# Optimization experiments

Measured on AMD Instinct MI355X. Metric: run time of the kernel, lower is better.

The kernel has to match this reference:

```python
import jax, jax.numpy as jnp
import numpy as np

N = 50000
E = 800000
NEG_SLOPE = 0.2
BN_EPS = 1e-5


def _bn(x, g, b, m, v):
    # BatchNorm1d in eval mode (running stats)
    return (x - m) * (g * jax.lax.rsqrt(v + BN_EPS)) + b


def _gat_conv(x, src, dst, W, a_src, a_dst, bias, heads, hid):
    n = x.shape[0]
    h = (x @ W).reshape(n, heads, hid)                      # [N,H,D]
    s_src = jnp.sum(h * a_src, axis=-1)                     # [N,H]
    s_dst = jnp.sum(h * a_dst, axis=-1)                     # [N,H]
    score = jax.nn.leaky_relu(s_src[src] + s_dst[dst], NEG_SLOPE)  # [E,H]
    # segment softmax over incoming edges of each dst node, per head
    mx = jax.ops.segment_max(score, dst, num_segments=n)
    ex = jnp.exp(score - mx[dst])
    sm = jax.ops.segment_sum(ex, dst, num_segments=n)
    alpha = ex / sm[dst]                                    # [E,H]
    msg = h[src] * alpha[:, :, None]                        # [E,H,D]
    out = jax.ops.segment_sum(msg, dst, num_segments=n)     # [N,H,D]
    return out.reshape(n, heads * hid) + bias


def setup_inputs() -> dict:
    key = jax.random.key(0)
    ks = jax.random.split(key, 16)
    d_in, heads, hid = 64, 8, 32
    wdim = heads * hid  # 256
    inp = {
        "x": jax.random.normal(ks[0], (N, d_in), jnp.float32),
        "edge_index": jax.random.randint(ks[1], (2, E), 0, N, jnp.int32),
        "bn1_g": jnp.ones((d_in,), jnp.float32),
        "bn1_b": jnp.zeros((d_in,), jnp.float32),
        "bn1_m": jnp.zeros((d_in,), jnp.float32),
        "bn1_v": jnp.ones((d_in,), jnp.float32),
        "W1": jax.random.normal(ks[2], (d_in, wdim), jnp.float32) * (1.0 / np.sqrt(d_in)),
        "a1_src": jax.random.normal(ks[3], (heads, hid), jnp.float32) * 0.1,
        "a1_dst": jax.random.normal(ks[4], (heads, hid), jnp.float32) * 0.1,
        "b1": jnp.zeros((wdim,), jnp.float32),
        "bn2_g": jnp.ones((wdim,), jnp.float32),
        "bn2_b": jnp.zeros((wdim,), jnp.float32),
        "bn2_m": jnp.zeros((wdim,), jnp.float32),
        "bn2_v": jnp.ones((wdim,), jnp.float32),
        "W2": jax.random.normal(ks[5], (wdim, wdim), jnp.float32) * (1.0 / np.sqrt(wdim)),
        "a2_src": jax.random.normal(ks[6], (heads, hid), jnp.float32) * 0.1,
        "a2_dst": jax.random.normal(ks[7], (heads, hid), jnp.float32) * 0.1,
        "b2": jnp.zeros((wdim,), jnp.float32),
        "bn3_g": jnp.ones((wdim,), jnp.float32),
        "bn3_b": jnp.zeros((wdim,), jnp.float32),
        "bn3_m": jnp.zeros((wdim,), jnp.float32),
        "bn3_v": jnp.ones((wdim,), jnp.float32),
        "skip_W": jax.random.normal(ks[8], (d_in, wdim), jnp.float32) * (1.0 / np.sqrt(d_in)),
        "skip_b": jnp.zeros((wdim,), jnp.float32),
        "p1_W": jax.random.normal(ks[9], (wdim, hid), jnp.float32) * (1.0 / np.sqrt(wdim)),
        "p1_b": jnp.zeros((hid,), jnp.float32),
        "p2_W": jax.random.normal(ks[10], (hid, 1), jnp.float32) * (1.0 / np.sqrt(hid)),
        "p2_b": jnp.zeros((1,), jnp.float32),
    }
    return inp


def reference(x, edge_index, bn1_g, bn1_b, bn1_m, bn1_v, W1, a1_src, a1_dst, b1,
              bn2_g, bn2_b, bn2_m, bn2_v, W2, a2_src, a2_dst, b2,
              bn3_g, bn3_b, bn3_m, bn3_v, skip_W, skip_b, p1_W, p1_b, p2_W, p2_b):
    heads, hid = 8, 32
    n = x.shape[0]
    # add self loops once (PyG GATConv default add_self_loops=True)
    loops = jnp.arange(n, dtype=edge_index.dtype)
    src = jnp.concatenate([edge_index[0], loops])
    dst = jnp.concatenate([edge_index[1], loops])

    x_in = x
    h = _bn(x, bn1_g, bn1_b, bn1_m, bn1_v)
    h = jax.nn.elu(_gat_conv(h, src, dst, W1, a1_src, a1_dst, b1, heads, hid))
    h = _bn(h, bn2_g, bn2_b, bn2_m, bn2_v)
    h = jax.nn.elu(_gat_conv(h, src, dst, W2, a2_src, a2_dst, b2, heads, hid))
    h = _bn(h, bn3_g, bn3_b, bn3_m, bn3_v)
    h = h + (x_in @ skip_W + skip_b)
    h = jax.nn.relu(h @ p1_W + p1_b)
    return h @ p2_W + p2_b  # [N, 1]
```

## Files before the change

### kernel.cpp

```cpp
#include <hip/hip_runtime.h>
#include <hip/hip_bf16.h>
#include <math.h>
#include <stdint.h>

#define HID 256
#define HEADS 8
#define BN_EPS 1e-5f
#define NEG 0.2f
#define WCAP 96
#define SEPT 8
#define SCHUNK (256 * SEPT)

typedef _Float16 hv8 __attribute__((ext_vector_type(8)));
typedef float f32x4 __attribute__((ext_vector_type(4)));

__device__ __forceinline__ float lrelu(float x) { return x > 0.f ? x : NEG * x; }
__device__ __forceinline__ float eluf(float x)  { return x > 0.f ? x : expm1f(x); }

__device__ __forceinline__ unsigned short f2h(float f) {
    _Float16 h = (_Float16)f;
    union { _Float16 h; unsigned short u; } c; c.h = h;
    return c.u;
}
__device__ __forceinline__ float h2f(unsigned short u) {
    union { unsigned short u; _Float16 h; } c; c.u = u;
    return (float)c.h;
}
__device__ __forceinline__ unsigned int pk2h(float lo, float hi) {
    return (unsigned int)f2h(lo) | ((unsigned int)f2h(hi) << 16);
}

#define FMAMIX_LO(acc, pk, al) \
    asm("v_fma_mix_f32 %0, %1, %2, %0 op_sel:[0,0,0] op_sel_hi:[1,0,0]" \
        : "+v"(acc) : "v"(pk), "v"(al))
#define FMAMIX_HI(acc, pk, al) \
    asm("v_fma_mix_f32 %0, %1, %2, %0 op_sel:[1,0,0] op_sel_hi:[1,0,0]" \
        : "+v"(acc) : "v"(pk), "v"(al))


__global__ __launch_bounds__(256) void degree_kernel(const int* __restrict__ ei,
                                                     int* __restrict__ deg,
                                                     int E, int EE) {
    int e = blockIdx.x * 256 + threadIdx.x;
    if (e >= EE) return;
    int d = (e < E) ? ei[E + e] : (e - E);
    atomicAdd(&deg[d], 1);
}

__global__ __launch_bounds__(256) void scan1_kernel(const int* __restrict__ deg,
                                                    int* __restrict__ bsum, int N) {
    __shared__ int part[256];
    int t = threadIdx.x;
    int base = blockIdx.x * SCHUNK + t * SEPT;
    int s = 0;
    if (base + SEPT <= N) {
        int4 a = *(const int4*)&deg[base];
        int4 c = *(const int4*)&deg[base + 4];
        s = a.x + a.y + a.z + a.w + c.x + c.y + c.z + c.w;
    } else {
#pragma unroll
        for (int i = 0; i < SEPT; ++i) {
            int j = base + i;
            if (j < N) s += deg[j];
        }
    }
    part[t] = s;
    __syncthreads();
    for (int d = 128; d > 0; d >>= 1) {
        if (t < d) part[t] += part[t + d];
        __syncthreads();
    }
    if (t == 0) bsum[blockIdx.x] = part[0];
}

__global__ __launch_bounds__(256) void scan2_kernel(int* __restrict__ bsum,
                                                    int* __restrict__ offs,
                                                    int nb, int N) {
    __shared__ int part[256];
    int t = threadIdx.x;
    int v = (t < nb) ? bsum[t] : 0;
    part[t] = v;
    __syncthreads();
    for (int d = 1; d < 256; d <<= 1) {
        int o = (t >= d) ? part[t - d] : 0;
        __syncthreads();
        part[t] += o;
        __syncthreads();
    }
    if (t < nb) bsum[t] = part[t] - v;
    if (t == 255) offs[N] = part[255];
}

__global__ __launch_bounds__(256) void scan3_kernel(const int* __restrict__ deg,
                                                    const int* __restrict__ bsum,
                                                    int* __restrict__ offs, int N) {
    __shared__ int part[256];
    int t = threadIdx.x;
    int base = blockIdx.x * SCHUNK + t * SEPT;
    int loc[SEPT];
    int s = 0;
#pragma unroll
    for (int i = 0; i < SEPT; ++i) {
        int j = base + i;
        int d = (j < N) ? deg[j] : 0;
        loc[i] = s;
        s += d;
    }
    part[t] = s;
    __syncthreads();
    for (int d = 1; d < 256; d <<= 1) {
        int o = (t >= d) ? part[t - d] : 0;
        __syncthreads();
        part[t] += o;
        __syncthreads();
    }
    int ex = part[t] - s + bsum[blockIdx.x];
#pragma unroll
    for (int i = 0; i < SEPT; ++i) {
        int j = base + i;
        if (j < N) offs[j] = ex + loc[i];
    }
}

__global__ __launch_bounds__(256) void scatter_kernel(const int* __restrict__ ei,
                                                      const int* __restrict__ offs,
                                                      int* __restrict__ cur,
                                                      int* __restrict__ csr_src,
                                                      int E, int EE) {
    int e = blockIdx.x * 256 + threadIdx.x;
    if (e >= EE) return;
    int s = (e < E) ? ei[e] : (e - E);
    int d = (e < E) ? ei[E + e] : (e - E);
    int pos = offs[d] + atomicAdd(&cur[d], 1);
    csr_src[pos] = s;
}

__device__ __forceinline__ void wfrag_body(const float* __restrict__ W,
                                           const float* __restrict__ g,
                                           const float* __restrict__ v,
                                           unsigned short* __restrict__ frag,
                                           int tile, int l) {
    int ct = tile & 15, kt = tile >> 4;
    int c = ct * 16 + (l & 15);
    int k0 = kt * 32 + (l >> 4) * 8;
    float val[8];
#pragma unroll
    for (int j = 0; j < 8; ++j) {
        float s = g[k0 + j] * rsqrtf(v[k0 + j] + BN_EPS);
        val[j] = W[(size_t)(k0 + j) * HID + c] * s;
    }
    uint4 o;
    o.x = pk2h(val[0], val[1]);
    o.y = pk2h(val[2], val[3]);
    o.z = pk2h(val[4], val[5]);
    o.w = pk2h(val[6], val[7]);
    *(uint4*)&frag[((size_t)tile * 64 + l) * 8] = o;
}

__global__ __launch_bounds__(256) void prep_kernel(
    const float* __restrict__ W1, const float* __restrict__ bn1_g,
    const float* __restrict__ bn1_b, const float* __restrict__ bn1_m,
    const float* __restrict__ bn1_v,
    const float* __restrict__ W2, const float* __restrict__ bn2_g,
    const float* __restrict__ bn2_b, const float* __restrict__ bn2_m,
    const float* __restrict__ bn2_v,
    const float* __restrict__ g3, const float* __restrict__ b3,
    const float* __restrict__ m3, const float* __restrict__ v3,
    const float* __restrict__ skip_W, const float* __restrict__ skip_b,
    const float* __restrict__ p1_W, const float* __restrict__ p1_b,
    unsigned short* __restrict__ wf1, unsigned short* __restrict__ wf2,
    unsigned short* __restrict__ hf, float* __restrict__ c1,
    float* __restrict__ c2, float* __restrict__ cp) {
    int b = blockIdx.x;
    int tid = threadIdx.x;
    int sub = tid >> 6, l = tid & 63;

    if (b < 8) {
        wfrag_body(W1, bn1_g, bn1_v, wf1, b * 4 + sub, l);
    } else if (b < 40) {
        wfrag_body(W2, bn2_g, bn2_v, wf2, (b - 8) * 4 + sub, l);
    } else if (b < 45) {
        int tile = (b - 40) * 4 + sub;
        int mt = tile & 1, kt = tile >> 1;
        int j = mt * 16 + (l & 15);
        int k0 = kt * 32 + (l >> 4) * 8;
        float val[8];
#pragma unroll
        for (int jj = 0; jj < 8; ++jj) {
            int c = k0 + jj;
            if (c < HID) {
                float s3 = g3[c] * rsqrtf(v3[c] + BN_EPS);
                val[jj] = s3 * p1_W[c * 32 + j];
            } else {
                float acc = 0.f;
                for (int cc = 0; cc < HID; ++cc)
                    acc = fmaf(skip_W[(size_t)(c - HID) * HID + cc],
                               p1_W[cc * 32 + j], acc);
                val[jj] = acc;
            }
        }
        uint4 o;
        o.x = pk2h(val[0], val[1]);
        o.y = pk2h(val[2], val[3]);
        o.z = pk2h(val[4], val[5]);
        o.w = pk2h(val[6], val[7]);
        *(uint4*)&hf[((size_t)tile * 64 + l) * 8] = o;
    } else if (b == 45) {
        float acc = 0.f;
        for (int k = 0; k < 64; ++k) {
            float s = bn1_g[k] * rsqrtf(bn1_v[k] + BN_EPS);
            acc = fmaf(bn1_b[k] - bn1_m[k] * s, W1[(size_t)k * HID + tid], acc);
        }
        c1[tid] = acc;
    } else if (b == 46) {
        float acc = 0.f;
        for (int k = 0; k < HID; ++k) {
            float s = bn2_g[k] * rsqrtf(bn2_v[k] + BN_EPS);
            acc = fmaf(bn2_b[k] - bn2_m[k] * s, W2[(size_t)k * HID + tid], acc);
        }
        c2[tid] = acc;
    } else {
        if (tid < 32) {
            float acc = p1_b[tid];
            for (int c = 0; c < HID; ++c) {
                float s3 = g3[c] * rsqrtf(v3[c] + BN_EPS);
                acc = fmaf(b3[c] - m3[c] * s3 + skip_b[c], p1_W[c * 32 + tid], acc);
            }
            cp[tid] = acc;
        }
    }
}

template <int K, bool F16IN>
__global__ __launch_bounds__(256) void gemm_mfma(
    const float* __restrict__ inf, const unsigned short* __restrict__ inh,
    const unsigned short* __restrict__ wfrag, const float* __restrict__ cvec,
    const float* __restrict__ a_src, const float* __restrict__ a_dst,
    unsigned short* __restrict__ h, float* __restrict__ s_src,
    float* __restrict__ s_dst, int N) {
    constexpr int KT = K / 32;
    constexpr int OPR = K / 8;
    __shared__ unsigned short xfrag[KT * 4 * 64 * 8];
    int tid = threadIdx.x;
    int w = tid >> 6, l = tid & 63;
    int gg = l >> 4, li = l & 15;
    int base = blockIdx.x * 64;

    for (int id = tid; id < 64 * OPR; id += 256) {
        int r = id / OPR, o = id % OPR;
        int node = min(base + r, N - 1);
        uint4 pkv;
        if constexpr (F16IN) {
            pkv = *(const uint4*)&inh[(size_t)node * K + o * 8];
        } else {
            const float* p = &inf[(size_t)node * K + o * 8];
            float4 f0 = *(const float4*)p;
            float4 f1 = *(const float4*)(p + 4);
            pkv.x = pk2h(f0.x, f0.y);
            pkv.y = pk2h(f0.z, f0.w);
            pkv.z = pk2h(f1.x, f1.y);
            pkv.w = pk2h(f1.z, f1.w);
        }
        int kt = o >> 2, og = o & 3, nt = r >> 4;
        *(uint4*)&xfrag[(((kt * 4 + nt) * 64) + (r & 15) + 16 * og) * 8] = pkv;
    }
    __syncthreads();

    f32x4 acc[4][4];
#pragma unroll
    for (int mm = 0; mm < 4; ++mm) {
        float4 cv = *(const float4*)&cvec[64 * w + 16 * mm + 4 * gg];
#pragma unroll
        for (int nn = 0; nn < 4; ++nn) {
            acc[mm][nn][0] = cv.x; acc[mm][nn][1] = cv.y;
            acc[mm][nn][2] = cv.z; acc[mm][nn][3] = cv.w;
        }
    }

    for (int ks = 0; ks < KT; ++ks) {
        hv8 a[4], b[4];
#pragma unroll
        for (int mm = 0; mm < 4; ++mm)
            a[mm] = *(const hv8*)&wfrag[((size_t)(ks * 16 + w * 4 + mm) * 64 + l) * 8];
#pragma unroll
        for (int nn = 0; nn < 4; ++nn)
            b[nn] = *(const hv8*)&xfrag[((ks * 4 + nn) * 64 + l) * 8];
#pragma unroll
        for (int mm = 0; mm < 4; ++mm)
#pragma unroll
            for (int nn = 0; nn < 4; ++nn)
                acc[mm][nn] = __builtin_amdgcn_mfma_f32_16x16x32_f16(
                    a[mm], b[nn], acc[mm][nn], 0, 0, 0);
    }

    float svp[4][2], sdp[4][2];
#pragma unroll
    for (int nn = 0; nn < 4; ++nn) { svp[nn][0]=0.f; svp[nn][1]=0.f; sdp[nn][0]=0.f; sdp[nn][1]=0.f; }

#pragma unroll
    for (int mm = 0; mm < 4; ++mm) {
        int cb = 64 * w + 16 * mm + 4 * gg;
        float4 as4 = *(const float4*)&a_src[cb];
        float4 ad4 = *(const float4*)&a_dst[cb];
        int hp = mm >> 1;
#pragma unroll
        for (int nn = 0; nn < 4; ++nn) {
            f32x4 A = acc[mm][nn];
            svp[nn][hp] += A[0]*as4.x + A[1]*as4.y + A[2]*as4.z + A[3]*as4.w;
            sdp[nn][hp] += A[0]*ad4.x + A[1]*ad4.y + A[2]*ad4.z + A[3]*ad4.w;
            int node = base + 16 * nn + li;
            if (node < N) {
                ushort4 pkv;
                pkv.x = f2h(A[0]); pkv.y = f2h(A[1]);
                pkv.z = f2h(A[2]); pkv.w = f2h(A[3]);
                *(ushort4*)&h[(size_t)node * HID + cb] = pkv;
            }
        }
    }
#pragma unroll
    for (int nn = 0; nn < 4; ++nn)
#pragma unroll
        for (int hp = 0; hp < 2; ++hp) {
            svp[nn][hp] += __shfl_xor(svp[nn][hp], 16);
            svp[nn][hp] += __shfl_xor(svp[nn][hp], 32);
            sdp[nn][hp] += __shfl_xor(sdp[nn][hp], 16);
            sdp[nn][hp] += __shfl_xor(sdp[nn][hp], 32);
        }
    if (gg == 0) {
#pragma unroll
        for (int nn = 0; nn < 4; ++nn) {
            int node = base + 16 * nn + li;
            if (node < N) {
#pragma unroll
                for (int hp = 0; hp < 2; ++hp) {
                    s_src[node * HEADS + 2 * w + hp] = svp[nn][hp];
                    s_dst[node * HEADS + 2 * w + hp] = sdp[nn][hp];
                }
            }
        }
    }
}

__global__ __launch_bounds__(256) void agg_kernel(
    const unsigned short* __restrict__ h, const float* __restrict__ s_src,
    const float* __restrict__ s_dst, const int* __restrict__ offs,
    const int* __restrict__ csr_src, const float* __restrict__ bias,
    unsigned short* __restrict__ outp, int N) {
    __shared__ float al_lds[4][WCAP][8];
    __shared__ int   u_lds[4][WCAP];
    __shared__ float mi_lds[4][16];
    int tid = threadIdx.x;
    int w = tid >> 6, l = tid & 63;
    int vtx = blockIdx.x * 4 + w;
    if (vtx >= N) return;
    int beg = offs[vtx], end = offs[vtx + 1];
    int deg = end - beg;
    int dc = min(deg, WCAP);

    int headA = l & 7, slot = l >> 3;
    float sdv = s_dst[vtx * HEADS + headA];

    float m = -3.0e38f;
    for (int e = slot; e < deg; e += 8) {
        int u = csr_src[beg + e];
        float sc = lrelu(s_src[u * HEADS + headA] + sdv);
        if (e < WCAP) {
            if (headA == 0) u_lds[w][e] = u;
            al_lds[w][e][headA] = sc;
        }
        m = fmaxf(m, sc);
    }
    m = fmaxf(m, __shfl_xor(m, 8));
    m = fmaxf(m, __shfl_xor(m, 16));
    m = fmaxf(m, __shfl_xor(m, 32));

    float s = 0.f;
    for (int e = slot; e < dc; e += 8) {
        float p = __expf(al_lds[w][e][headA] - m);
        al_lds[w][e][headA] = p;
        s += p;
    }
    for (int e = WCAP + slot; e < deg; e += 8) {
        int u = csr_src[beg + e];
        s += __expf(lrelu(s_src[u * HEADS + headA] + sdv) - m);
    }
    s += __shfl_xor(s, 8);
    s += __shfl_xor(s, 16);
    s += __shfl_xor(s, 32);
    if (slot == 0) {
        mi_lds[w][headA] = m;
        mi_lds[w][8 + headA] = 1.f / s;
    }
    __builtin_amdgcn_wave_barrier();

    int grp = l >> 5, gl = l & 31;
    int hd = gl >> 2;
    float a0 = 0.f, a1 = 0.f, a2 = 0.f, a3 = 0.f;
    float a4 = 0.f, a5 = 0.f, a6 = 0.f, a7 = 0.f;
#pragma unroll 2
    for (int e = grp; e < dc; e += 2) {
        int u = u_lds[w][e];
        float al = al_lds[w][e][hd];
        uint4 hv = *(const uint4*)&h[(size_t)u * HID + 8 * gl];
        FMAMIX_LO(a0, hv.x, al); FMAMIX_HI(a1, hv.x, al);
        FMAMIX_LO(a2, hv.y, al); FMAMIX_HI(a3, hv.y, al);
        FMAMIX_LO(a4, hv.z, al); FMAMIX_HI(a5, hv.z, al);
        FMAMIX_LO(a6, hv.w, al); FMAMIX_HI(a7, hv.w, al);
    }
    if (deg > WCAP) {
        float mh = mi_lds[w][hd];
        float sdh = s_dst[vtx * HEADS + hd];
        for (int e = WCAP + grp; e < deg; e += 2) {
            int u = csr_src[beg + e];
            float al = __expf(lrelu(s_src[u * HEADS + hd] + sdh) - mh);
            uint4 hv = *(const uint4*)&h[(size_t)u * HID + 8 * gl];
            FMAMIX_LO(a0, hv.x, al); FMAMIX_HI(a1, hv.x, al);
            FMAMIX_LO(a2, hv.y, al); FMAMIX_HI(a3, hv.y, al);
            FMAMIX_LO(a4, hv.z, al); FMAMIX_HI(a5, hv.z, al);
            FMAMIX_LO(a6, hv.w, al); FMAMIX_HI(a7, hv.w, al);
        }
    }
    a0 += __shfl_xor(a0, 32); a1 += __shfl_xor(a1, 32);
    a2 += __shfl_xor(a2, 32); a3 += __shfl_xor(a3, 32);
    a4 += __shfl_xor(a4, 32); a5 += __shfl_xor(a5, 32);
    a6 += __shfl_xor(a6, 32); a7 += __shfl_xor(a7, 32);
    if (grp == 0) {
        float inv = mi_lds[w][8 + hd];
        float4 b0 = *(const float4*)&bias[8 * gl];
        float4 b1 = *(const float4*)&bias[8 * gl + 4];
        uint4 ov;
        ov.x = pk2h(eluf(a0 * inv + b0.x), eluf(a1 * inv + b0.y));
        ov.y = pk2h(eluf(a2 * inv + b0.z), eluf(a3 * inv + b0.w));
        ov.z = pk2h(eluf(a4 * inv + b1.x), eluf(a5 * inv + b1.y));
        ov.w = pk2h(eluf(a6 * inv + b1.z), eluf(a7 * inv + b1.w));
        *(uint4*)&outp[(size_t)vtx * HID + 8 * gl] = ov;
    }
}

__global__ __launch_bounds__(256) void final_mfma(
    const unsigned short* __restrict__ t_in, const float* __restrict__ x,
    const unsigned short* __restrict__ hf, const float* __restrict__ cp,
    const float* __restrict__ p2_W, const float* __restrict__ p2_b,
    float* __restrict__ outp, int N) {
    constexpr int KT = 10;
    __shared__ unsigned short xfrag[KT * 4 * 64 * 8];
    int tid = threadIdx.x;
    int w = tid >> 6, l = tid & 63;
    int gg = l >> 4, li = l & 15;
    int base = blockIdx.x * 64;

    for (int id = tid; id < 64 * 40; id += 256) {
        int r = id / 40, o = id % 40;
        int node = min(base + r, N - 1);
        uint4 pkv;
        if (o < 32) {
            pkv = *(const uint4*)&t_in[(size_t)node * HID + o * 8];
        } else {
            const float* p = &x[(size_t)node * 64 + (o - 32) * 8];
            float4 f0 = *(const float4*)p;
            float4 f1 = *(const float4*)(p + 4);
            pkv.x = pk2h(f0.x, f0.y);
            pkv.y = pk2h(f0.z, f0.w);
            pkv.z = pk2h(f1.x, f1.y);
            pkv.w = pk2h(f1.z, f1.w);
        }
        int kt = o >> 2, og = o & 3, nt = r >> 4;
        *(uint4*)&xfrag[(((kt * 4 + nt) * 64) + (r & 15) + 16 * og) * 8] = pkv;
    }
    __syncthreads();

    f32x4 acc[2];
#pragma unroll
    for (int mt = 0; mt < 2; ++mt) {
        float4 cv = *(const float4*)&cp[mt * 16 + 4 * gg];
        acc[mt][0] = cv.x; acc[mt][1] = cv.y; acc[mt][2] = cv.z; acc[mt][3] = cv.w;
    }

    for (int kt = 0; kt < KT; ++kt) {
        hv8 b = *(const hv8*)&xfrag[((kt * 4 + w) * 64 + l) * 8];
#pragma unroll
        for (int mt = 0; mt < 2; ++mt) {
            hv8 a = *(const hv8*)&hf[((size_t)(kt * 2 + mt) * 64 + l) * 8];
            acc[mt] = __builtin_amdgcn_mfma_f32_16x16x32_f16(a, b, acc[mt], 0, 0, 0);
        }
    }

    float po = 0.f;
#pragma unroll
    for (int mt = 0; mt < 2; ++mt) {
        float4 p2v = *(const float4*)&p2_W[mt * 16 + 4 * gg];
        po += fmaxf(acc[mt][0], 0.f) * p2v.x;
        po += fmaxf(acc[mt][1], 0.f) * p2v.y;
        po += fmaxf(acc[mt][2], 0.f) * p2v.z;
        po += fmaxf(acc[mt][3], 0.f) * p2v.w;
    }
    po += __shfl_xor(po, 16);
    po += __shfl_xor(po, 32);
    int node = base + 16 * w + li;
    if (gg == 0 && node < N) outp[node] = po + p2_b[0];
}


extern "C" void kernel_launch(void* const* d_in, const int* in_sizes, int n_in,
                              void* d_out, int out_size, void* d_ws, size_t ws_size,
                              hipStream_t stream) {
    const float* x      = (const float*)d_in[0];
    const int*   ei     = (const int*)  d_in[1];
    const float* bn1_g  = (const float*)d_in[2];
    const float* bn1_b  = (const float*)d_in[3];
    const float* bn1_m  = (const float*)d_in[4];
    const float* bn1_v  = (const float*)d_in[5];
    const float* W1     = (const float*)d_in[6];
    const float* a1_src = (const float*)d_in[7];
    const float* a1_dst = (const float*)d_in[8];
    const float* b1     = (const float*)d_in[9];
    const float* bn2_g  = (const float*)d_in[10];
    const float* bn2_b  = (const float*)d_in[11];
    const float* bn2_m  = (const float*)d_in[12];
    const float* bn2_v  = (const float*)d_in[13];
    const float* W2     = (const float*)d_in[14];
    const float* a2_src = (const float*)d_in[15];
    const float* a2_dst = (const float*)d_in[16];
    const float* b2     = (const float*)d_in[17];
    const float* bn3_g  = (const float*)d_in[18];
    const float* bn3_b  = (const float*)d_in[19];
    const float* bn3_m  = (const float*)d_in[20];
    const float* bn3_v  = (const float*)d_in[21];
    const float* skip_W = (const float*)d_in[22];
    const float* skip_b = (const float*)d_in[23];
    const float* p1_W   = (const float*)d_in[24];
    const float* p1_b   = (const float*)d_in[25];
    const float* p2_W   = (const float*)d_in[26];
    const float* p2_b   = (const float*)d_in[27];

    int N = in_sizes[0] / 64;
    int E = in_sizes[1] / 2;
    int EE = E + N;

    uintptr_t w = (uintptr_t)d_ws;
    auto carve = [&](size_t bytes) -> void* {
        uintptr_t p = w;
        w += (bytes + 255) & ~(size_t)255;
        return (void*)p;
    };
    int*   deg  = (int*)carve((size_t)N * 4);
    int*   cur  = (int*)carve((size_t)N * 4);
    int*   offs = (int*)carve(((size_t)N + 1) * 4);
    int*   csr  = (int*)carve((size_t)EE * 4);
    int*   bsum = (int*)carve((size_t)256 * 4);
    float* ssrc = (float*)carve((size_t)N * HEADS * 4);
    float* sdst = (float*)carve((size_t)N * HEADS * 4);
    unsigned short* wf1 = (unsigned short*)carve((size_t)2 * 16 * 64 * 8 * 2);
    unsigned short* wf2 = (unsigned short*)carve((size_t)8 * 16 * 64 * 8 * 2);
    unsigned short* hf  = (unsigned short*)carve((size_t)20 * 64 * 8 * 2);
    float* c1   = (float*)carve((size_t)HID * 4);
    float* c2   = (float*)carve((size_t)HID * 4);
    float* cp   = (float*)carve((size_t)32 * 4);
    unsigned short* hbf = (unsigned short*)carve((size_t)N * HID * 2);
    unsigned short* tbuf = (unsigned short*)carve((size_t)N * HID * 2);

    hipMemsetAsync(deg, 0, ((size_t)N * 4 + 255 & ~(size_t)255) + (size_t)N * 4, stream);

    prep_kernel<<<48, 256, 0, stream>>>(
        W1, bn1_g, bn1_b, bn1_m, bn1_v,
        W2, bn2_g, bn2_b, bn2_m, bn2_v,
        bn3_g, bn3_b, bn3_m, bn3_v, skip_W, skip_b, p1_W, p1_b,
        wf1, wf2, hf, c1, c2, cp);

    int eblk = (EE + 255) / 256;
    int nb = (N + SCHUNK - 1) / SCHUNK;
    degree_kernel<<<eblk, 256, 0, stream>>>(ei, deg, E, EE);
    scan1_kernel<<<nb, 256, 0, stream>>>(deg, bsum, N);
    scan2_kernel<<<1, 256, 0, stream>>>(bsum, offs, nb, N);
    scan3_kernel<<<nb, 256, 0, stream>>>(deg, bsum, offs, N);
    scatter_kernel<<<eblk, 256, 0, stream>>>(ei, offs, cur, csr, E, EE);

    int gblk = (N + 63) / 64;
    int ablk = (N + 3) / 4;
    gemm_mfma<64, false><<<gblk, 256, 0, stream>>>(x, nullptr, wf1, c1,
                                                   a1_src, a1_dst,
                                                   hbf, ssrc, sdst, N);
    agg_kernel<<<ablk, 256, 0, stream>>>(hbf, ssrc, sdst, offs, csr, b1, tbuf, N);

    gemm_mfma<HID, true><<<gblk, 256, 0, stream>>>(nullptr, tbuf, wf2, c2,
                                                   a2_src, a2_dst,
                                                   hbf, ssrc, sdst, N);
    agg_kernel<<<ablk, 256, 0, stream>>>(hbf, ssrc, sdst, offs, csr, b2, tbuf, N);

    final_mfma<<<gblk, 256, 0, stream>>>(tbuf, x, hf, cp, p2_W, p2_b,
                                         (float*)d_out, N);
}
```

Baseline: 337.4 us.

## Merge degree count into prep kernel, unroll aggregation gathers, use packed RTZ conversions

The degree-counting atomics move into extra blocks of the prep kernel, which removes one kernel launch. The aggregation loop is unrolled to issue four independent neighbour row gathers per iteration for more memory-level parallelism. The epilogue now splits the output write across both half-wave groups, so no lanes sit idle. Float-to-half packing uses the packed round-toward-zero conversion instead of separate converts, and ELU uses __expf minus one. These lower instruction count but change rounding slightly (RTZ instead of RNE, and less accurate expm1 near zero).

```diff
diff --git a/kernel.cpp b/kernel.cpp
--- a/kernel.cpp
+++ b/kernel.cpp
@@ -12,22 +12,24 @@
 #define SCHUNK (256 * SEPT)
 
 typedef _Float16 hv8 __attribute__((ext_vector_type(8)));
+typedef __fp16 fv2 __attribute__((ext_vector_type(2)));
 typedef float f32x4 __attribute__((ext_vector_type(4)));
 
 __device__ __forceinline__ float lrelu(float x) { return x > 0.f ? x : NEG * x; }
-__device__ __forceinline__ float eluf(float x)  { return x > 0.f ? x : expm1f(x); }
+__device__ __forceinline__ float eluf(float x)  { return x > 0.f ? x : __expf(x) - 1.f; }
 
 __device__ __forceinline__ unsigned short f2h(float f) {
     _Float16 h = (_Float16)f;
     union { _Float16 h; unsigned short u; } c; c.h = h;
     return c.u;
 }
-__device__ __forceinline__ float h2f(unsigned short u) {
-    union { unsigned short u; _Float16 h; } c; c.u = u;
-    return (float)c.h;
-}
 __device__ __forceinline__ unsigned int pk2h(float lo, float hi) {
     return (unsigned int)f2h(lo) | ((unsigned int)f2h(hi) << 16);
+}
+__device__ __forceinline__ unsigned int pkrtz(float lo, float hi) {
+    fv2 r = __builtin_amdgcn_cvt_pkrtz(lo, hi);
+    union { fv2 h; unsigned int u; } c; c.h = r;
+    return c.u;
 }
 
 #define FMAMIX_LO(acc, pk, al) \
@@ -36,16 +38,12 @@
 #define FMAMIX_HI(acc, pk, al) \
     asm("v_fma_mix_f32 %0, %1, %2, %0 op_sel:[1,0,0] op_sel_hi:[1,0,0]" \
         : "+v"(acc) : "v"(pk), "v"(al))
-
-
-__global__ __launch_bounds__(256) void degree_kernel(const int* __restrict__ ei,
-                                                     int* __restrict__ deg,
-                                                     int E, int EE) {
-    int e = blockIdx.x * 256 + threadIdx.x;
-    if (e >= EE) return;
-    int d = (e < E) ? ei[E + e] : (e - E);
-    atomicAdd(&deg[d], 1);
-}
+#define FMAMIX4(q, al) \
+    FMAMIX_LO(a0, q.x, al); FMAMIX_HI(a1, q.x, al); \
+    FMAMIX_LO(a2, q.y, al); FMAMIX_HI(a3, q.y, al); \
+    FMAMIX_LO(a4, q.z, al); FMAMIX_HI(a5, q.z, al); \
+    FMAMIX_LO(a6, q.w, al); FMAMIX_HI(a7, q.w, al)
+
 
 __global__ __launch_bounds__(256) void scan1_kernel(const int* __restrict__ deg,
                                                     int* __restrict__ bsum, int N) {
@@ -170,11 +168,21 @@
     const float* __restrict__ p1_W, const float* __restrict__ p1_b,
     unsigned short* __restrict__ wf1, unsigned short* __restrict__ wf2,
     unsigned short* __restrict__ hf, float* __restrict__ c1,
-    float* __restrict__ c2, float* __restrict__ cp) {
+    float* __restrict__ c2, float* __restrict__ cp,
+    const int* __restrict__ ei, int* __restrict__ deg, int E, int EE) {
     int b = blockIdx.x;
     int tid = threadIdx.x;
+
+    if (b >= 48) {
+        int e = (b - 48) * 256 + tid;
+        if (e < EE) {
+            int d = (e < E) ? ei[E + e] : (e - E);
+            atomicAdd(&deg[d], 1);
+        }
+        return;
+    }
+
     int sub = tid >> 6, l = tid & 63;
-
     if (b < 8) {
         wfrag_body(W1, bn1_g, bn1_v, wf1, b * 4 + sub, l);
     } else if (b < 40) {
@@ -256,10 +264,10 @@
             const float* p = &inf[(size_t)node * K + o * 8];
             float4 f0 = *(const float4*)p;
             float4 f1 = *(const float4*)(p + 4);
-            pkv.x = pk2h(f0.x, f0.y);
-            pkv.y = pk2h(f0.z, f0.w);
-            pkv.z = pk2h(f1.x, f1.y);
-            pkv.w = pk2h(f1.z, f1.w);
+            pkv.x = pkrtz(f0.x, f0.y);
+            pkv.y = pkrtz(f0.z, f0.w);
+            pkv.z = pkrtz(f1.x, f1.y);
+            pkv.w = pkrtz(f1.z, f1.w);
         }
         int kt = o >> 2, og = o & 3, nt = r >> 4;
         *(uint4*)&xfrag[(((kt * 4 + nt) * 64) + (r & 15) + 16 * og) * 8] = pkv;
@@ -310,10 +318,10 @@
             sdp[nn][hp] += A[0]*ad4.x + A[1]*ad4.y + A[2]*ad4.z + A[3]*ad4.w;
             int node = base + 16 * nn + li;
             if (node < N) {
-                ushort4 pkv;
-                pkv.x = f2h(A[0]); pkv.y = f2h(A[1]);
-                pkv.z = f2h(A[2]); pkv.w = f2h(A[3]);
-                *(ushort4*)&h[(size_t)node * HID + cb] = pkv;
+                uint2 pkv2;
+                pkv2.x = pkrtz(A[0], A[1]);
+                pkv2.y = pkrtz(A[2], A[3]);
+                *(uint2*)&h[(size_t)node * HID + cb] = pkv2;
             }
         }
     }
@@ -397,44 +405,57 @@
     int hd = gl >> 2;
     float a0 = 0.f, a1 = 0.f, a2 = 0.f, a3 = 0.f;
     float a4 = 0.f, a5 = 0.f, a6 = 0.f, a7 = 0.f;
-#pragma unroll 2
-    for (int e = grp; e < dc; e += 2) {
-        int u = u_lds[w][e];
-        float al = al_lds[w][e][hd];
-        uint4 hv = *(const uint4*)&h[(size_t)u * HID + 8 * gl];
-        FMAMIX_LO(a0, hv.x, al); FMAMIX_HI(a1, hv.x, al);
-        FMAMIX_LO(a2, hv.y, al); FMAMIX_HI(a3, hv.y, al);
-        FMAMIX_LO(a4, hv.z, al); FMAMIX_HI(a5, hv.z, al);
-        FMAMIX_LO(a6, hv.w, al); FMAMIX_HI(a7, hv.w, al);
+    const unsigned short* hb = h + 8 * gl;
+    int e = grp;
+    for (; e + 6 < dc; e += 8) {
+        int u0 = u_lds[w][e];
+        int u1 = u_lds[w][e + 2];
+        int u2 = u_lds[w][e + 4];
+        int u3 = u_lds[w][e + 6];
+        float l0 = al_lds[w][e][hd];
+        float l1 = al_lds[w][e + 2][hd];
+        float l2 = al_lds[w][e + 4][hd];
+        float l3 = al_lds[w][e + 6][hd];
+        uint4 v0 = *(const uint4*)&hb[(size_t)u0 * HID];
+        uint4 v1 = *(const uint4*)&hb[(size_t)u1 * HID];
+        uint4 v2 = *(const uint4*)&hb[(size_t)u2 * HID];
+        uint4 v3 = *(const uint4*)&hb[(size_t)u3 * HID];
+        FMAMIX4(v0, l0);
+        FMAMIX4(v1, l1);
+        FMAMIX4(v2, l2);
+        FMAMIX4(v3, l3);
+    }
+    for (; e < dc; e += 2) {
+        int u0 = u_lds[w][e];
+        float l0 = al_lds[w][e][hd];
+        uint4 v0 = *(const uint4*)&hb[(size_t)u0 * HID];
+        FMAMIX4(v0, l0);
     }
     if (deg > WCAP) {
         float mh = mi_lds[w][hd];
         float sdh = s_dst[vtx * HEADS + hd];
-        for (int e = WCAP + grp; e < deg; e += 2) {
-            int u = csr_src[beg + e];
+        for (int ee = WCAP + grp; ee < deg; ee += 2) {
+            int u = csr_src[beg + ee];
             float al = __expf(lrelu(s_src[u * HEADS + hd] + sdh) - mh);
-            uint4 hv = *(const uint4*)&h[(size_t)u * HID + 8 * gl];
-            FMAMIX_LO(a0, hv.x, al); FMAMIX_HI(a1, hv.x, al);
-            FMAMIX_LO(a2, hv.y, al); FMAMIX_HI(a3, hv.y, al);
-            FMAMIX_LO(a4, hv.z, al); FMAMIX_HI(a5, hv.z, al);
-            FMAMIX_LO(a6, hv.w, al); FMAMIX_HI(a7, hv.w, al);
+            uint4 v0 = *(const uint4*)&hb[(size_t)u * HID];
+            FMAMIX4(v0, al);
         }
     }
     a0 += __shfl_xor(a0, 32); a1 += __shfl_xor(a1, 32);
     a2 += __shfl_xor(a2, 32); a3 += __shfl_xor(a3, 32);
     a4 += __shfl_xor(a4, 32); a5 += __shfl_xor(a5, 32);
     a6 += __shfl_xor(a6, 32); a7 += __shfl_xor(a7, 32);
-    if (grp == 0) {
-        float inv = mi_lds[w][8 + hd];
-        float4 b0 = *(const float4*)&bias[8 * gl];
-        float4 b1 = *(const float4*)&bias[8 * gl + 4];
-        uint4 ov;
-        ov.x = pk2h(eluf(a0 * inv + b0.x), eluf(a1 * inv + b0.y));
-        ov.y = pk2h(eluf(a2 * inv + b0.z), eluf(a3 * inv + b0.w));
-        ov.z = pk2h(eluf(a4 * inv + b1.x), eluf(a5 * inv + b1.y));
-        ov.w = pk2h(eluf(a6 * inv + b1.z), eluf(a7 * inv + b1.w));
-        *(uint4*)&outp[(size_t)vtx * HID + 8 * gl] = ov;
-    }
+
+    float inv = mi_lds[w][8 + hd];
+    float e0 = grp ? a4 : a0;
+    float e1 = grp ? a5 : a1;
+    float e2 = grp ? a6 : a2;
+    float e3 = grp ? a7 : a3;
+    float4 bb = *(const float4*)&bias[8 * gl + 4 * grp];
+    uint2 ov;
+    ov.x = pkrtz(eluf(e0 * inv + bb.x), eluf(e1 * inv + bb.y));
+    ov.y = pkrtz(eluf(e2 * inv + bb.z), eluf(e3 * inv + bb.w));
+    *(uint2*)&outp[(size_t)vtx * HID + 8 * gl + 4 * grp] = ov;
 }
 
 __global__ __launch_bounds__(256) void final_mfma(
@@ -459,10 +480,10 @@
             const float* p = &x[(size_t)node * 64 + (o - 32) * 8];
             float4 f0 = *(const float4*)p;
             float4 f1 = *(const float4*)(p + 4);
-            pkv.x = pk2h(f0.x, f0.y);
-            pkv.y = pk2h(f0.z, f0.w);
-            pkv.z = pk2h(f1.x, f1.y);
-            pkv.w = pk2h(f1.z, f1.w);
+            pkv.x = pkrtz(f0.x, f0.y);
+            pkv.y = pkrtz(f0.z, f0.w);
+            pkv.z = pkrtz(f1.x, f1.y);
+            pkv.w = pkrtz(f1.z, f1.w);
         }
         int kt = o >> 2, og = o & 3, nt = r >> 4;
         *(uint4*)&xfrag[(((kt * 4 + nt) * 64) + (r & 15) + 16 * og) * 8] = pkv;
@@ -561,15 +582,14 @@
 
     hipMemsetAsync(deg, 0, ((size_t)N * 4 + 255 & ~(size_t)255) + (size_t)N * 4, stream);
 
-    prep_kernel<<<48, 256, 0, stream>>>(
+    int eblk = (EE + 255) / 256;
+    prep_kernel<<<48 + eblk, 256, 0, stream>>>(
         W1, bn1_g, bn1_b, bn1_m, bn1_v,
         W2, bn2_g, bn2_b, bn2_m, bn2_v,
         bn3_g, bn3_b, bn3_m, bn3_v, skip_W, skip_b, p1_W, p1_b,
-        wf1, wf2, hf, c1, c2, cp);
-
-    int eblk = (EE + 255) / 256;
+        wf1, wf2, hf, c1, c2, cp, ei, deg, E, EE);
+
     int nb = (N + SCHUNK - 1) / SCHUNK;
-    degree_kernel<<<eblk, 256, 0, stream>>>(ei, deg, E, EE);
     scan1_kernel<<<nb, 256, 0, stream>>>(deg, bsum, N);
     scan2_kernel<<<1, 256, 0, stream>>>(bsum, offs, nb, N);
     scan3_kernel<<<nb, 256, 0, stream>>>(deg, bsum, offs, N);
```

Measured after the change: 319.2 us. -5.4%, faster.
